# Optimization experiments

Measured on AMD Instinct MI355X. Metric: run time of the kernel, lower is better.

## Reference

```python
import jax, jax.numpy as jnp
import numpy as np

EPS = 1e-6
NEG = -1e9

def rotate_half(x):
    x1, x2 = jnp.split(x, 2, axis=-1)
    return jnp.concatenate([-x2, x1], axis=-1)

def setup_inputs() -> dict:
    key = jax.random.key(0)
    ks = jax.random.split(key, 5)
    T, d_model, n_h = 2048, 2048, 16
    d_h = d_model // n_h
    x = jax.random.normal(ks[0], (T, d_model), dtype=jnp.float32)
    # RoPE tables (realistic rotary angles)
    inv_freq = 1.0 / (10000.0 ** (jnp.arange(0, d_h, 2, dtype=jnp.float32) / d_h))
    t = jnp.arange(T, dtype=jnp.float32)
    freqs = jnp.einsum('t,f->tf', t, inv_freq)
    emb = jnp.concatenate([freqs, freqs], axis=-1)  # [T, d_h]
    cos, sin = jnp.cos(emb), jnp.sin(emb)
    attention_mask = jnp.ones((T,), dtype=bool)
    ln_w = jnp.ones((d_model,), dtype=jnp.float32)
    w_qkv = jax.random.normal(ks[1], (3 * d_model, d_model), dtype=jnp.float32) / np.sqrt(d_model)
    w_o = jax.random.normal(ks[2], (d_model, d_model), dtype=jnp.float32) / np.sqrt(d_model)
    return {"x": x, "cos": cos, "sin": sin, "attention_mask": attention_mask,
            "ln_w": ln_w, "w_qkv": w_qkv, "w_o": w_o}

def reference(x, cos, sin, attention_mask, ln_w, w_qkv, w_o):
    T, d_model = x.shape
    n_h = 16
    d_h = d_model // n_h
    scale = 1.0 / np.sqrt(d_h)
    # RMSNorm
    ms = jnp.mean(x * x, axis=-1, keepdims=True)
    h = ln_w * x * jax.lax.rsqrt(ms + EPS)
    # fused QKV projection (eqx Linear: y = W @ x => h @ W.T)
    qkv = (h @ w_qkv.T).reshape(T, 3, n_h, d_h)
    q = qkv[:, 0].transpose(1, 0, 2)  # [H, T, d_h]
    k = qkv[:, 1].transpose(1, 0, 2)
    v = qkv[:, 2].transpose(1, 0, 2)
    # RoPE (cos/sin broadcast over heads)
    q = q * cos + rotate_half(q) * sin
    k = k * cos + rotate_half(k) * sin
    # attention scores with causal + padding mask
    scores = jnp.einsum('hqd,hkd->hqk', q, k) * scale
    causal = jnp.tril(jnp.ones((T, T), dtype=bool))[None]
    am = attention_mask.astype(bool)
    valid = causal & am[None, None, :]
    scores = jnp.where(valid, scores, NEG)
    scores = jnp.where(am[None, :, None], scores, NEG)
    probs = jax.nn.softmax(scores, axis=-1)
    out = jnp.einsum('hqk,hkd->hqd', probs, v)  # [H, T, d_h]
    out = out.transpose(1, 0, 2).reshape(T, d_model)
    out = out @ w_o.T
    out = jnp.where(attention_mask[:, None], out, 0.0)
    return x + out
```

## Files before the change

kernel.cpp:

```cpp
#include <hip/hip_runtime.h>


#define T_SEQ 2048
#define DM 2048
#define NH 16
#define DH 128
#define DM3 6144
#define TD (T_SEQ*DH)

typedef short s16x8 __attribute__((ext_vector_type(8)));
typedef float f32x4 __attribute__((ext_vector_type(4)));

static __device__ __forceinline__ unsigned short f2bf(float f){
  unsigned u = __builtin_bit_cast(unsigned, f);
  u += 0x7FFFu + ((u>>16)&1u);
  return (unsigned short)(u>>16);
}
static __device__ __forceinline__ float bf2f(unsigned short b){
  return __builtin_bit_cast(float, ((unsigned)b)<<16);
}
static __device__ __forceinline__ unsigned pk2bf(float a, float b){
  return (unsigned)f2bf(a) | ((unsigned)f2bf(b) << 16);
}
static __device__ __forceinline__ void gload_lds16(const void* g, void* l){
  __builtin_amdgcn_global_load_lds((const __attribute__((address_space(1))) void*)g,
                                   (__attribute__((address_space(3))) void*)l, 16, 0, 0);
}

__global__ __launch_bounds__(256) void cast_kernel(const float4* __restrict__ wq,
                                                   const float4* __restrict__ wo,
                                                   ushort4* __restrict__ wqo,
                                                   ushort4* __restrict__ woo,
                                                   int nq4, int ntot4){
  int i = blockIdx.x*256 + threadIdx.x;
  if (i >= ntot4) return;
  float4 v;
  if (i < nq4) v = wq[i]; else v = wo[i - nq4];
  ushort4 o; o.x=f2bf(v.x); o.y=f2bf(v.y); o.z=f2bf(v.z); o.w=f2bf(v.w);
  if (i < nq4) wqo[i] = o; else woo[i - nq4] = o;
}

__global__ __launch_bounds__(256) void rmsnorm_kernel(const float* __restrict__ x,
                                                      const float* __restrict__ w,
                                                      unsigned short* __restrict__ h){
  int row = blockIdx.x;
  int tid = threadIdx.x;
  const float4* xr = (const float4*)(x + (size_t)row*DM);
  float4 v0 = xr[tid], v1 = xr[tid+256];
  float ss = v0.x*v0.x+v0.y*v0.y+v0.z*v0.z+v0.w*v0.w
           + v1.x*v1.x+v1.y*v1.y+v1.z*v1.z+v1.w*v1.w;
  #pragma unroll
  for (int off=32; off; off>>=1) ss += __shfl_xor(ss, off, 64);
  __shared__ float wsum[4];
  if ((tid&63)==0) wsum[tid>>6] = ss;
  __syncthreads();
  float rs = rsqrtf((wsum[0]+wsum[1]+wsum[2]+wsum[3]) * (1.0f/DM) + 1e-6f);
  const float4* w4 = (const float4*)w;
  float4 wa = w4[tid], wb = w4[tid+256];
  ushort4* h4 = (ushort4*)(h + (size_t)row*DM);
  ushort4 o0, o1;
  o0.x=f2bf(v0.x*wa.x*rs); o0.y=f2bf(v0.y*wa.y*rs); o0.z=f2bf(v0.z*wa.z*rs); o0.w=f2bf(v0.w*wa.w*rs);
  o1.x=f2bf(v1.x*wb.x*rs); o1.y=f2bf(v1.y*wb.y*rs); o1.z=f2bf(v1.z*wb.z*rs); o1.w=f2bf(v1.w*wb.w*rs);
  h4[tid] = o0; h4[tid+256] = o1;
}

template <typename OUTT>
__global__ __launch_bounds__(256) void gemm_bt(const unsigned short* __restrict__ A,
                                               const unsigned short* __restrict__ B,
                                               OUTT* __restrict__ C,
                                               const float* __restrict__ resid,
                                               int M, int N, int K){
  __shared__ __align__(16) unsigned short As[128*32];
  __shared__ __align__(16) unsigned short Bs[128*32];
  int tid = threadIdx.x, lane = tid&63, wid = tid>>6;
  int c16 = lane&15, g = lane>>4;
  int bm = blockIdx.y, bn = blockIdx.x;
  int wr = wid>>1, wc = wid&1;
  f32x4 acc[4][4] = {};
  int nk = K >> 5;
  const char* Ab = (const char*)A;
  const char* Bb = (const char*)B;
  for (int ko=0; ko<nk; ++ko){
    #pragma unroll
    for (int c=0;c<2;c++){
      int li = (wid*2+c)*1024 + lane*16;
      int row = li>>6, colb = li&63;
      gload_lds16(Ab + ((size_t)(bm*128+row)*K + ko*32)*2 + colb,
                  (char*)As + (wid*2+c)*1024);
      gload_lds16(Bb + ((size_t)(bn*128+row)*K + ko*32)*2 + colb,
                  (char*)Bs + (wid*2+c)*1024);
    }
    __syncthreads();
    s16x8 af[4], bfr[4];
    #pragma unroll
    for (int m=0;m<4;m++) af[m]  = *(const s16x8*)&As[(wr*64+m*16+c16)*32 + g*8];
    #pragma unroll
    for (int n=0;n<4;n++) bfr[n] = *(const s16x8*)&Bs[(wc*64+n*16+c16)*32 + g*8];
    #pragma unroll
    for (int m=0;m<4;m++)
      #pragma unroll
      for (int n=0;n<4;n++)
        acc[m][n] = __builtin_amdgcn_mfma_f32_16x16x32_bf16(af[m], bfr[n], acc[m][n], 0,0,0);
    __syncthreads();
  }
  #pragma unroll
  for (int m=0;m<4;m++)
    #pragma unroll
    for (int n=0;n<4;n++){
      int r0 = bm*128 + wr*64 + m*16 + g*4;
      int c0 = bn*128 + wc*64 + n*16 + c16;
      #pragma unroll
      for (int r=0;r<4;r++){
        float v = acc[m][n][r];
        if (resid) v += resid[(size_t)(r0+r)*N + c0];
        if constexpr (__is_same(OUTT, float))
          C[(size_t)(r0+r)*N + c0] = v;
        else
          C[(size_t)(r0+r)*N + c0] = f2bf(v);
      }
    }
}

__global__ __launch_bounds__(256) void rope_kernel(const unsigned short* __restrict__ qkv,
                                                   const float* __restrict__ cs,
                                                   const float* __restrict__ sn,
                                                   unsigned short* __restrict__ Qr,
                                                   unsigned short* __restrict__ Kp){
  int idx = blockIdx.x*256 + threadIdx.x;
  int dh = idx & 63;
  int h  = (idx>>6) & (NH-1);
  int t  = idx >> 10;
  size_t base = (size_t)t*DM3 + h*DH;
  float c = cs[t*DH + dh], s = sn[t*DH + dh];
  float q1 = bf2f(qkv[base+dh]),      q2 = bf2f(qkv[base+dh+64]);
  float k1 = bf2f(qkv[base+DM+dh]),   k2 = bf2f(qkv[base+DM+dh+64]);
  const float sc = 0.088388347648318447f;
  size_t ob = ((size_t)h*T_SEQ + t)*DH + dh;
  Qr[ob]    = f2bf((q1*c - q2*s)*sc);
  Qr[ob+64] = f2bf((q2*c + q1*s)*sc);
  int b = t >> 5, r32 = t & 31;
  int n   = (r32>>2) & 1;
  int c16 = (r32&3) | ((r32>>3)<<2);
  int g = (dh>>3)&3, e = dh&7;
  int kk  = dh>>5;
  int kk2 = 2 + kk;
  size_t hb = (size_t)h*TD;
  int slot = ((g*16+c16)<<3) + e;
  Kp[hb + (size_t)((b*8 + n*4 + kk )*512 + slot)] = f2bf(k1*c - k2*s);
  Kp[hb + (size_t)((b*8 + n*4 + kk2)*512 + slot)] = f2bf(k2*c + k1*s);
}

__global__ __launch_bounds__(256) void vtrans_kernel(const unsigned short* __restrict__ qkv,
                                                     unsigned short* __restrict__ Vp){
  __shared__ unsigned short tile[32][33];
  int t0 = blockIdx.x*32, d0 = blockIdx.y*32, h = blockIdx.z;
  int c = threadIdx.x & 31, r0 = threadIdx.x >> 5;
  #pragma unroll
  for (int i=0;i<4;i++){
    int r = r0 + i*8;
    tile[r][c] = qkv[(size_t)(t0+r)*DM3 + 2*DM + h*DH + d0 + c];
  }
  __syncthreads();
  int w = threadIdx.x;
  if (w < 128){
    int n2l = w>>6, lane = w&63;
    int cc = lane&15, gg = lane>>4;
    union { unsigned short u[8]; s16x8 v; } ov;
    #pragma unroll
    for (int e=0;e<8;e++) ov.u[e] = tile[gg*8+e][n2l*16+cc];
    size_t dst = (size_t)h*TD + (size_t)(((t0>>5)*8 + (d0>>4) + n2l)*512 + lane*8);
    *(s16x8*)&Vp[dst] = ov.v;
  }
}

__global__ __launch_bounds__(256) void attn_kernel(const unsigned short* __restrict__ Qr,
                                                   const unsigned short* __restrict__ Kp,
                                                   const unsigned short* __restrict__ Vp,
                                                   unsigned short* __restrict__ O){
  __shared__ float sm[4][16];
  __shared__ float sl[4][16];
  __shared__ __align__(16) unsigned short so[4][16][128];
  int tid = threadIdx.x;
  int lane = tid & 63, wid = tid >> 6;
  int c16 = lane & 15, g = lane >> 4;
  int id = blockIdx.x;
  int h  = id & 15;
  int qt = 127 - (id >> 4);
  int qr0 = qt * 16;
  const unsigned short* Qh  = Qr + (size_t)h*TD;
  const unsigned short* Kph = Kp + (size_t)h*TD;
  const unsigned short* Vph = Vp + (size_t)h*TD;
  s16x8 aq[4];
  #pragma unroll
  for (int kk=0;kk<4;kk++)
    aq[kk] = *(const s16x8*)&Qh[(size_t)(qr0+c16)*DH + kk*32 + g*8];
  f32x4 o[8] = {};
  float m_q = -1e30f, l_q = 0.f;
  int nkv = (qr0 + 47) >> 5;
  int it0 = (wid*nkv) >> 2, it1 = ((wid+1)*nkv) >> 2;
  for (int it = it0; it < it1; ++it){
    int kv0 = it * 32;
    int cb = it * 8;
    f32x4 sf[2] = {};
    #pragma unroll
    for (int n=0;n<2;n++)
      #pragma unroll
      for (int kk=0;kk<4;kk++){
        s16x8 bk = *(const s16x8*)&Kph[(size_t)((cb + n*4 + kk)*512) + lane*8];
        sf[n] = __builtin_amdgcn_mfma_f32_16x16x32_bf16(bk, aq[kk], sf[n], 0,0,0);
      }
    if (kv0 + 31 > qr0){
      #pragma unroll
      for (int n=0;n<2;n++)
        #pragma unroll
        for (int r=0;r<4;r++)
          if (kv0 + 8*g + 4*n + r > qr0 + c16) sf[n][r] = -1e30f;
    }
    float mx = fmaxf(fmaxf(fmaxf(sf[0][0],sf[0][1]), fmaxf(sf[0][2],sf[0][3])),
                     fmaxf(fmaxf(sf[1][0],sf[1][1]), fmaxf(sf[1][2],sf[1][3])));
    mx = fmaxf(mx, __shfl_xor(mx, 16));
    mx = fmaxf(mx, __shfl_xor(mx, 32));
    if (!__all(mx - m_q <= 8.f)){
      float mnew = fmaxf(m_q, mx);
      float sc = __expf(m_q - mnew);
      m_q = mnew;
      float scr[4];
      #pragma unroll
      for (int r=0;r<4;r++) scr[r] = __shfl(sc, g*4 + r);
      #pragma unroll
      for (int n2=0;n2<8;n2++)
        #pragma unroll
        for (int r=0;r<4;r++) o[n2][r] *= scr[r];
      l_q *= sc;
    }
    float p[8];
    #pragma unroll
    for (int n=0;n<2;n++)
      #pragma unroll
      for (int r=0;r<4;r++) p[4*n+r] = __expf(sf[n][r] - m_q);
    float rs = ((p[0]+p[1])+(p[2]+p[3])) + ((p[4]+p[5])+(p[6]+p[7]));
    rs += __shfl_xor(rs, 16);
    rs += __shfl_xor(rs, 32);
    l_q += rs;
    union { unsigned u[4]; s16x8 v; } pau;
    pau.u[0] = pk2bf(p[0],p[1]); pau.u[1] = pk2bf(p[2],p[3]);
    pau.u[2] = pk2bf(p[4],p[5]); pau.u[3] = pk2bf(p[6],p[7]);
    #pragma unroll
    for (int n2=0;n2<8;n2++){
      s16x8 bv = *(const s16x8*)&Vph[(size_t)((cb + n2)*512) + lane*8];
      o[n2] = __builtin_amdgcn_mfma_f32_16x16x32_bf16(pau.v, bv, o[n2], 0,0,0);
    }
  }
  if (lane < 16){ sm[wid][lane] = m_q; sl[wid][lane] = l_q; }
  #pragma unroll
  for (int n2=0;n2<8;n2++)
    #pragma unroll
    for (int r=0;r<4;r++)
      so[wid][g*4+r][n2*16+c16] = f2bf(o[n2][r]);
  __syncthreads();
  int row = tid >> 4;
  int col = (tid & 15) * 8;
  float mg = fmaxf(fmaxf(sm[0][row], sm[1][row]), fmaxf(sm[2][row], sm[3][row]));
  float lg = 0.f;
  float acc[8] = {};
  #pragma unroll
  for (int w=0;w<4;w++){
    float e = __expf(sm[w][row] - mg);
    lg += sl[w][row] * e;
    #pragma unroll
    for (int j=0;j<8;j++) acc[j] += e * bf2f(so[w][row][col+j]);
  }
  float inv = 1.0f / lg;
  s16x8 ov;
  #pragma unroll
  for (int j=0;j<8;j++) ov[j] = (short)f2bf(acc[j]*inv);
  *(s16x8*)&O[(size_t)(qr0+row)*DM + h*DH + col] = ov;
}

extern "C" void kernel_launch(void* const* d_in, const int* in_sizes, int n_in,
                              void* d_out, int out_size, void* d_ws, size_t ws_size,
                              hipStream_t stream){
  const float* x    = (const float*)d_in[0];
  const float* cs   = (const float*)d_in[1];
  const float* sn   = (const float*)d_in[2];
  const float* ln_w = (const float*)d_in[4];
  const float* wqkv = (const float*)d_in[5];
  const float* wo   = (const float*)d_in[6];

  char* ws = (char*)d_ws;
  unsigned short* h     = (unsigned short*)(ws);
  unsigned short* wqkvb = (unsigned short*)(ws + 8388608);
  unsigned short* wob   = (unsigned short*)(ws + 33554432);
  unsigned short* qkv   = (unsigned short*)(ws + 41943040);
  unsigned short* attno = qkv;
  unsigned short* Qr    = (unsigned short*)(ws + 67108864);
  unsigned short* Kp    = (unsigned short*)(ws + 75497472);
  unsigned short* Vp    = (unsigned short*)(ws + 83886080);
  float* out            = (float*)d_out;

  cast_kernel<<<16384, 256, 0, stream>>>((const float4*)wqkv, (const float4*)wo,
                                         (ushort4*)wqkvb, (ushort4*)wob,
                                         3145728, 4194304);
  rmsnorm_kernel<<<2048, 256, 0, stream>>>(x, ln_w, h);
  gemm_bt<unsigned short><<<dim3(48,16), 256, 0, stream>>>(h, wqkvb, qkv, nullptr, 2048, 6144, 2048);
  rope_kernel<<<8192, 256, 0, stream>>>(qkv, cs, sn, Qr, Kp);
  vtrans_kernel<<<dim3(64,4,16), 256, 0, stream>>>(qkv, Vp);
  attn_kernel<<<dim3(2048), 256, 0, stream>>>(Qr, Kp, Vp, attno);
  gemm_bt<float><<<dim3(16,16), 256, 0, stream>>>(attno, wob, out, x, 2048, 2048, 2048);
}
```

Measured before the change: 327.4 us.

## Assign each attention wave its own query tile instead of splitting KV range

The attention kernel previously had four waves share one 16-row query tile, each covering a quarter of the KV range, then merged partial softmax states through shared memory with a barrier. Now each wave owns a distinct query tile, walks the full causal KV range, and normalizes and writes its output directly. The grid drops from 2048 to 512 blocks. This removes the LDS merge, the barrier and the extra exp work, but lowers block count and makes waves within a block finish at different times because their causal lengths differ. The output stores also become scattered 2-byte writes instead of 16-byte vectors.

```diff
diff --git a/kernel.cpp b/kernel.cpp
--- a/kernel.cpp
+++ b/kernel.cpp
@@ -177,15 +177,13 @@
                                                    const unsigned short* __restrict__ Kp,
                                                    const unsigned short* __restrict__ Vp,
                                                    unsigned short* __restrict__ O){
-  __shared__ float sm[4][16];
-  __shared__ float sl[4][16];
-  __shared__ __align__(16) unsigned short so[4][16][128];
   int tid = threadIdx.x;
   int lane = tid & 63, wid = tid >> 6;
   int c16 = lane & 15, g = lane >> 4;
   int id = blockIdx.x;
   int h  = id & 15;
-  int qt = 127 - (id >> 4);
+  int qg = 31 - (id >> 4);
+  int qt = qg*4 + wid;
   int qr0 = qt * 16;
   const unsigned short* Qh  = Qr + (size_t)h*TD;
   const unsigned short* Kph = Kp + (size_t)h*TD;
@@ -197,8 +195,7 @@
   f32x4 o[8] = {};
   float m_q = -1e30f, l_q = 0.f;
   int nkv = (qr0 + 47) >> 5;
-  int it0 = (wid*nkv) >> 2, it1 = ((wid+1)*nkv) >> 2;
-  for (int it = it0; it < it1; ++it){
+  for (int it = 0; it < nkv; ++it){
     int kv0 = it * 32;
     int cb = it * 8;
     f32x4 sf[2] = {};
@@ -251,30 +248,15 @@
       o[n2] = __builtin_amdgcn_mfma_f32_16x16x32_bf16(pau.v, bv, o[n2], 0,0,0);
     }
   }
-  if (lane < 16){ sm[wid][lane] = m_q; sl[wid][lane] = l_q; }
+  float il = 1.0f / l_q;
+  float linv[4];
+  #pragma unroll
+  for (int r=0;r<4;r++) linv[r] = __shfl(il, g*4 + r);
   #pragma unroll
   for (int n2=0;n2<8;n2++)
     #pragma unroll
     for (int r=0;r<4;r++)
-      so[wid][g*4+r][n2*16+c16] = f2bf(o[n2][r]);
-  __syncthreads();
-  int row = tid >> 4;
-  int col = (tid & 15) * 8;
-  float mg = fmaxf(fmaxf(sm[0][row], sm[1][row]), fmaxf(sm[2][row], sm[3][row]));
-  float lg = 0.f;
-  float acc[8] = {};
-  #pragma unroll
-  for (int w=0;w<4;w++){
-    float e = __expf(sm[w][row] - mg);
-    lg += sl[w][row] * e;
-    #pragma unroll
-    for (int j=0;j<8;j++) acc[j] += e * bf2f(so[w][row][col+j]);
-  }
-  float inv = 1.0f / lg;
-  s16x8 ov;
-  #pragma unroll
-  for (int j=0;j<8;j++) ov[j] = (short)f2bf(acc[j]*inv);
-  *(s16x8*)&O[(size_t)(qr0+row)*DM + h*DH + col] = ov;
+      O[(size_t)(qr0+g*4+r)*DM + h*DH + n2*16 + c16] = f2bf(o[n2][r]*linv[r]);
 }
 
 extern "C" void kernel_launch(void* const* d_in, const int* in_sizes, int n_in,
@@ -305,6 +287,6 @@
   gemm_bt<unsigned short><<<dim3(48,16), 256, 0, stream>>>(h, wqkvb, qkv, nullptr, 2048, 6144, 2048);
   rope_kernel<<<8192, 256, 0, stream>>>(qkv, cs, sn, Qr, Kp);
   vtrans_kernel<<<dim3(64,4,16), 256, 0, stream>>>(qkv, Vp);
-  attn_kernel<<<dim3(2048), 256, 0, stream>>>(Qr, Kp, Vp, attno);
+  attn_kernel<<<dim3(512), 256, 0, stream>>>(Qr, Kp, Vp, attno);
   gemm_bt<float><<<dim3(16,16), 256, 0, stream>>>(attno, wob, out, x, 2048, 2048, 2048);
 }
```

Measured after the change: 476.0 us. 1.45x slower.
